# Kernel optimization log

Measured on AMD Instinct MI355X. Metric: run time of the kernel, lower is better.

## Reference

```python
import jax, jax.numpy as jnp
import numpy as np

# PyTorch LSTM cell with zero initial (h, c): W_hh @ h0 == 0, and c = sigmoid(i)*tanh(g)
# since the forget-gate term f*c0 vanishes. Gate order in torch: i, f, g, o.
# b here is the combined b_ih + b_hh (identical math).

def lstm_step0(x, Wih, b):
    pre = x @ Wih.T + b                      # (N, 4H)
    i, f, g, o = jnp.split(pre, 4, axis=-1)
    c = jax.nn.sigmoid(i) * jnp.tanh(g)
    return jax.nn.sigmoid(o) * jnp.tanh(c)   # (N, H)


def setup_inputs() -> dict:
    key = jax.random.key(0)
    ks = jax.random.split(key, 13)
    num_ts, num_periods, F = 128, 256, 128
    GH, NH, NF = 512, 256, 10
    s = lambda k, shape, fan: (jax.random.normal(k, shape, jnp.float32) / np.sqrt(fan))
    return {
        "X": jax.random.normal(ks[0], (num_ts, num_periods, F), jnp.float32),
        "g_Wih0": s(ks[1], (4 * GH, F), F),
        "g_b0": s(ks[2], (4 * GH,), GH),
        "g_Wih1": s(ks[3], (4 * GH, GH), GH),
        "g_b1": s(ks[4], (4 * GH,), GH),
        "aff_W": s(ks[5], (NF, GH), GH),
        "aff_b": s(ks[6], (NF,), GH),
        "n_Wih0": s(ks[7], (4 * NH, F), F),
        "n_b0": s(ks[8], (4 * NH,), NH),
        "n_Wih1": s(ks[9], (4 * NH, NH), NH),
        "n_b1": s(ks[10], (4 * NH,), NH),
        "noise_W": s(ks[11], (1, NH), NH),
        "noise_b": s(ks[12], (1,), NH),
    }


def reference(X, g_Wih0, g_b0, g_Wih1, g_b1, aff_W, aff_b,
              n_Wih0, n_b0, n_Wih1, n_b1, noise_W, noise_b):
    num_ts, num_periods, num_feats = X.shape
    x = X.reshape(-1, num_feats)             # (num_ts*num_periods, F)

    # Global factor branch: 2-layer LSTM single step from zero state
    hg = lstm_step0(lstm_step0(x, g_Wih0, g_b0), g_Wih1, g_b1)
    hg = jax.nn.relu(hg)
    mus = (hg @ aff_W.T + aff_b).sum(axis=-1).reshape(num_ts, num_periods)

    # Noise branch: 2-layer LSTM single step from zero state
    hn = lstm_step0(lstm_step0(x, n_Wih0, n_b0), n_Wih1, n_b1)
    hn = jax.nn.relu(hn)
    sigmas = jax.nn.softplus(hn @ noise_W.T + noise_b)  # log(1+exp(.)), stable
    sigmas = sigmas.reshape(num_ts, num_periods) + 1e-6
    return mus, sigmas
```

## Files before the change

kernel.cpp:

```cpp
#include <hip/hip_runtime.h>
#include <hip/hip_bf16.h>
#include <hip/hip_fp16.h>

typedef _Float16 h8_t __attribute__((ext_vector_type(8)));
typedef _Float16 h4_t __attribute__((ext_vector_type(4)));
typedef float f4_t __attribute__((ext_vector_type(4)));

#define M_ROWS 32768

__device__ __forceinline__ void gload_lds16(const void* g, void* l) {
  __builtin_amdgcn_global_load_lds((const __attribute__((address_space(1))) void*)g,
                                   (__attribute__((address_space(3))) void*)l, 16, 0, 0);
}

__device__ __forceinline__ float sigmoid_f(float x) { return 1.f / (1.f + __expf(-x)); }
__device__ __forceinline__ float tanh_f(float x) { return 1.f - 2.f / (__expf(2.f * x) + 1.f); }

__global__ void cvt_f32_f16(const float* __restrict__ s, _Float16* __restrict__ d, int n) {
  int i = blockIdx.x * blockDim.x + threadIdx.x;
  int i4 = i * 4;
  if (i4 >= n) return;
  float4 v = *(const float4*)(s + i4);
  h4_t o;
  o[0] = (_Float16)v.x; o[1] = (_Float16)v.y; o[2] = (_Float16)v.z; o[3] = (_Float16)v.w;
  *(h4_t*)(d + i4) = o;
}

__global__ void prep_wsum(const float* __restrict__ aff_W, const float* __restrict__ aff_b,
                          float* __restrict__ wsum) {
  int j = threadIdx.x;
  float s = 0.f;
#pragma unroll
  for (int r = 0; r < 10; ++r) s += aff_W[r * 512 + j];
  wsum[j] = s;
  if (j == 0) {
    float bs = 0.f;
#pragma unroll
    for (int r = 0; r < 10; ++r) bs += aff_b[r];
    wsum[512] = bs;
  }
}

__global__ void zero2(float* __restrict__ pg, float* __restrict__ pn) {
  int i = blockIdx.x * blockDim.x + threadIdx.x;
  pg[i] = 0.f;
  pn[i] = 0.f;
}

template <int K_DIM, int H_DIM, bool FUSE>
__global__ __launch_bounds__(256, 2) void lstm_gemm(
    const _Float16* __restrict__ A,
    const _Float16* __restrict__ W,
    const float* __restrict__ bias,
    _Float16* __restrict__ Hout,
    const float* __restrict__ rvec,
    float* __restrict__ partial) {
  __shared__ __align__(16) _Float16 As[128 * 64];
  __shared__ __align__(16) _Float16 Bs[3 * 64 * 64];

  const int tid = threadIdx.x;
  const int wid = tid >> 6;
  const int lane = tid & 63;
  const int wave_m = wid >> 1;
  const int wave_h = wid & 1;
  const int q = lane >> 4;
  const int tcol = lane & 15;

  const int m0 = blockIdx.x * 128;
  const int h0 = blockIdx.y * 64;

  f4_t acc[3][4][2];
#pragma unroll
  for (int p = 0; p < 3; ++p)
#pragma unroll
    for (int mi = 0; mi < 4; ++mi)
#pragma unroll
      for (int ni = 0; ni < 2; ++ni) acc[p][mi][ni] = (f4_t){0.f, 0.f, 0.f, 0.f};

  for (int k0 = 0; k0 < K_DIM; k0 += 64) {
#pragma unroll
    for (int c = 0; c < 4; ++c) {
      int o = ((wid * 4 + c) << 10) + (lane << 4);
      int row = o >> 7;
      int kel = (o & 127) >> 1;
      gload_lds16(A + (size_t)(m0 + row) * K_DIM + k0 + kel, (char*)As + o);
    }
#pragma unroll
    for (int c = 0; c < 6; ++c) {
      int o = ((wid * 6 + c) << 10) + (lane << 4);
      int p = o >> 13;
      int oo = o & 8191;
      int j = oo >> 7;
      int kel = (oo & 127) >> 1;
      int grow = (p == 0 ? 0 : (p == 1 ? 2 * H_DIM : 3 * H_DIM)) + h0 + j;
      gload_lds16(W + (size_t)grow * K_DIM + k0 + kel, (char*)Bs + o);
    }
    __syncthreads();

#pragma unroll
    for (int ks = 0; ks < 2; ++ks) {
      h8_t af[4];
#pragma unroll
      for (int mi = 0; mi < 4; ++mi)
        af[mi] = *(const h8_t*)&As[(wave_m * 64 + mi * 16 + tcol) * 64 + ks * 32 + q * 8];
#pragma unroll
      for (int p = 0; p < 3; ++p) {
#pragma unroll
        for (int ni = 0; ni < 2; ++ni) {
          h8_t bf = *(const h8_t*)&Bs[p * 4096 + (wave_h * 32 + ni * 16 + tcol) * 64 + ks * 32 + q * 8];
#pragma unroll
          for (int mi = 0; mi < 4; ++mi)
            acc[p][mi][ni] = __builtin_amdgcn_mfma_f32_16x16x32_f16(af[mi], bf, acc[p][mi][ni], 0, 0, 0);
        }
      }
    }
    __syncthreads();
  }

  const int mrow0 = m0 + wave_m * 64;
  const int jcol0 = h0 + wave_h * 32;

  if constexpr (!FUSE) {
#pragma unroll
    for (int ni = 0; ni < 2; ++ni) {
      int j = jcol0 + ni * 16 + tcol;
      float bi = bias[j];
      float bg = bias[2 * H_DIM + j];
      float bo = bias[3 * H_DIM + j];
#pragma unroll
      for (int mi = 0; mi < 4; ++mi) {
#pragma unroll
        for (int r = 0; r < 4; ++r) {
          float pi = acc[0][mi][ni][r] + bi;
          float pgt = acc[1][mi][ni][r] + bg;
          float po = acc[2][mi][ni][r] + bo;
          float cc = sigmoid_f(pi) * tanh_f(pgt);
          float hh = sigmoid_f(po) * tanh_f(cc);
          int m = mrow0 + mi * 16 + q * 4 + r;
          Hout[(size_t)m * H_DIM + j] = (_Float16)hh;
        }
      }
    }
  } else {
    float rsum[4][4];
#pragma unroll
    for (int mi = 0; mi < 4; ++mi)
#pragma unroll
      for (int r = 0; r < 4; ++r) rsum[mi][r] = 0.f;
#pragma unroll
    for (int ni = 0; ni < 2; ++ni) {
      int j = jcol0 + ni * 16 + tcol;
      float bi = bias[j];
      float bg = bias[2 * H_DIM + j];
      float bo = bias[3 * H_DIM + j];
      float rv = rvec[j];
#pragma unroll
      for (int mi = 0; mi < 4; ++mi) {
#pragma unroll
        for (int r = 0; r < 4; ++r) {
          float pi = acc[0][mi][ni][r] + bi;
          float pgt = acc[1][mi][ni][r] + bg;
          float po = acc[2][mi][ni][r] + bo;
          float cc = sigmoid_f(pi) * tanh_f(pgt);
          float hh = sigmoid_f(po) * tanh_f(cc);
          hh = fmaxf(hh, 0.f);
          rsum[mi][r] += hh * rv;
        }
      }
    }
#pragma unroll
    for (int mi = 0; mi < 4; ++mi) {
#pragma unroll
      for (int r = 0; r < 4; ++r) {
        float v = rsum[mi][r];
        v += __shfl_xor(v, 1);
        v += __shfl_xor(v, 2);
        v += __shfl_xor(v, 4);
        v += __shfl_xor(v, 8);
        if (tcol == 0) atomicAdd(&partial[mrow0 + mi * 16 + q * 4 + r], v);
      }
    }
  }
}

__global__ void finalize(const float* __restrict__ pg, const float* __restrict__ pn,
                         const float* __restrict__ wsum, const float* __restrict__ noise_b,
                         float* __restrict__ out) {
  int i = blockIdx.x * blockDim.x + threadIdx.x;
  out[i] = pg[i] + wsum[512];
  float x = pn[i] + noise_b[0];
  float sp = fmaxf(x, 0.f) + log1pf(expf(-fabsf(x)));
  out[M_ROWS + i] = sp + 1e-6f;
}

extern "C" void kernel_launch(void* const* d_in, const int* in_sizes, int n_in,
                              void* d_out, int out_size, void* d_ws, size_t ws_size,
                              hipStream_t stream) {
  const float* X       = (const float*)d_in[0];
  const float* g_Wih0  = (const float*)d_in[1];
  const float* g_b0    = (const float*)d_in[2];
  const float* g_Wih1  = (const float*)d_in[3];
  const float* g_b1    = (const float*)d_in[4];
  const float* aff_W   = (const float*)d_in[5];
  const float* aff_b   = (const float*)d_in[6];
  const float* n_Wih0  = (const float*)d_in[7];
  const float* n_b0    = (const float*)d_in[8];
  const float* n_Wih1  = (const float*)d_in[9];
  const float* n_b1    = (const float*)d_in[10];
  const float* noise_W = (const float*)d_in[11];
  const float* noise_b = (const float*)d_in[12];
  float* out = (float*)d_out;

  char* w = (char*)d_ws;
  _Float16* Xh  = (_Float16*)w; w += (size_t)M_ROWS * 128 * 2;
  _Float16* Wg0 = (_Float16*)w; w += 2048 * 128 * 2;
  _Float16* Wg1 = (_Float16*)w; w += 2048 * 512 * 2;
  _Float16* Wn0 = (_Float16*)w; w += 1024 * 128 * 2;
  _Float16* Wn1 = (_Float16*)w; w += 1024 * 256 * 2;
  _Float16* h1g = (_Float16*)w; w += (size_t)M_ROWS * 512 * 2;
  _Float16* h1n = (_Float16*)w; w += (size_t)M_ROWS * 256 * 2;
  float* pg   = (float*)w; w += (size_t)M_ROWS * 4;
  float* pn   = (float*)w; w += (size_t)M_ROWS * 4;
  float* wsum = (float*)w; w += 4096;

  auto cvt = [&](const float* s, _Float16* d, int n) {
    cvt_f32_f16<<<(n / 4 + 255) / 256, 256, 0, stream>>>(s, d, n);
  };
  cvt(X, Xh, M_ROWS * 128);
  cvt(g_Wih0, Wg0, 2048 * 128);
  cvt(g_Wih1, Wg1, 2048 * 512);
  cvt(n_Wih0, Wn0, 1024 * 128);
  cvt(n_Wih1, Wn1, 1024 * 256);
  prep_wsum<<<1, 512, 0, stream>>>(aff_W, aff_b, wsum);
  zero2<<<M_ROWS / 256, 256, 0, stream>>>(pg, pn);

  lstm_gemm<128, 512, false><<<dim3(M_ROWS / 128, 8), 256, 0, stream>>>(Xh, Wg0, g_b0, h1g, nullptr, nullptr);
  lstm_gemm<128, 256, false><<<dim3(M_ROWS / 128, 4), 256, 0, stream>>>(Xh, Wn0, n_b0, h1n, nullptr, nullptr);
  lstm_gemm<512, 512, true><<<dim3(M_ROWS / 128, 8), 256, 0, stream>>>(h1g, Wg1, g_b1, nullptr, wsum, pg);
  lstm_gemm<256, 256, true><<<dim3(M_ROWS / 128, 4), 256, 0, stream>>>(h1n, Wn1, n_b1, nullptr, noise_W, pn);

  finalize<<<M_ROWS / 256, 256, 0, stream>>>(pg, pn, wsum, noise_b, out);
}
```

Baseline: 287.2 us.

## Fuse prep kernels, merge branch GEMMs per layer, swizzle LDS tiles

All preprocessing (f16 casts, accumulator zeroing, affine weight-sum) now runs in one kernel, and the global and noise LSTM GEMMs for each layer are merged into a single launch selected by blockIdx.y. LDS tiles get an XOR swizzle on 16-byte chunks to reduce bank conflicts on the MFMA operand reads. Global pointers are precomputed and bumped each step, and the K loop is fully unrolled. This cuts launch count and tail idle time and may improve LDS throughput, at the cost of more registers and branch divergence across blocks.

```diff
diff --git a/kernel.cpp b/kernel.cpp
--- a/kernel.cpp
+++ b/kernel.cpp
@@ -16,48 +16,59 @@
 __device__ __forceinline__ float sigmoid_f(float x) { return 1.f / (1.f + __expf(-x)); }
 __device__ __forceinline__ float tanh_f(float x) { return 1.f - 2.f / (__expf(2.f * x) + 1.f); }
 
-__global__ void cvt_f32_f16(const float* __restrict__ s, _Float16* __restrict__ d, int n) {
-  int i = blockIdx.x * blockDim.x + threadIdx.x;
-  int i4 = i * 4;
-  if (i4 >= n) return;
+struct GArgs {
+  const _Float16* A;
+  const _Float16* W;
+  const float* bias;
+  _Float16* Hout;
+  const float* rvec;
+  float* partial;
+};
+
+__global__ void prep_all(const float* __restrict__ X, const float* __restrict__ gW0,
+                         const float* __restrict__ gW1, const float* __restrict__ nW0,
+                         const float* __restrict__ nW1, const float* __restrict__ aff_W,
+                         const float* __restrict__ aff_b,
+                         _Float16* __restrict__ Xh, _Float16* __restrict__ Wg0,
+                         _Float16* __restrict__ Wg1, _Float16* __restrict__ Wn0,
+                         _Float16* __restrict__ Wn1,
+                         float* __restrict__ pg, float* __restrict__ pn,
+                         float* __restrict__ wsum) {
+  int b = blockIdx.x;
+  const float* s; _Float16* d; int base;
+  if (b < 4096)      { s = X;   d = Xh;  base = b; }
+  else if (b < 4352) { s = gW0; d = Wg0; base = b - 4096; }
+  else if (b < 5376) { s = gW1; d = Wg1; base = b - 4352; }
+  else if (b < 5504) { s = nW0; d = Wn0; base = b - 5376; }
+  else if (b < 5760) { s = nW1; d = Wn1; base = b - 5504; }
+  else if (b < 5888) {
+    int i = (b - 5760) * 256 + threadIdx.x;
+    pg[i] = 0.f; pn[i] = 0.f;
+    return;
+  } else {
+    int j = (b - 5888) * 256 + threadIdx.x;
+    float sum = 0.f;
+#pragma unroll
+    for (int r = 0; r < 10; ++r) sum += aff_W[r * 512 + j];
+    wsum[j] = sum;
+    if (j == 0) {
+      float bs = 0.f;
+#pragma unroll
+      for (int r = 0; r < 10; ++r) bs += aff_b[r];
+      wsum[512] = bs;
+    }
+    return;
+  }
+  int i4 = (base * 256 + threadIdx.x) * 4;
   float4 v = *(const float4*)(s + i4);
   h4_t o;
   o[0] = (_Float16)v.x; o[1] = (_Float16)v.y; o[2] = (_Float16)v.z; o[3] = (_Float16)v.w;
   *(h4_t*)(d + i4) = o;
 }
 
-__global__ void prep_wsum(const float* __restrict__ aff_W, const float* __restrict__ aff_b,
-                          float* __restrict__ wsum) {
-  int j = threadIdx.x;
-  float s = 0.f;
-#pragma unroll
-  for (int r = 0; r < 10; ++r) s += aff_W[r * 512 + j];
-  wsum[j] = s;
-  if (j == 0) {
-    float bs = 0.f;
-#pragma unroll
-    for (int r = 0; r < 10; ++r) bs += aff_b[r];
-    wsum[512] = bs;
-  }
-}
-
-__global__ void zero2(float* __restrict__ pg, float* __restrict__ pn) {
-  int i = blockIdx.x * blockDim.x + threadIdx.x;
-  pg[i] = 0.f;
-  pn[i] = 0.f;
-}
-
 template <int K_DIM, int H_DIM, bool FUSE>
-__global__ __launch_bounds__(256, 2) void lstm_gemm(
-    const _Float16* __restrict__ A,
-    const _Float16* __restrict__ W,
-    const float* __restrict__ bias,
-    _Float16* __restrict__ Hout,
-    const float* __restrict__ rvec,
-    float* __restrict__ partial) {
-  __shared__ __align__(16) _Float16 As[128 * 64];
-  __shared__ __align__(16) _Float16 Bs[3 * 64 * 64];
-
+__device__ __forceinline__ void gemm_body(const GArgs& ga, int h0,
+                                          _Float16* As, _Float16* Bs) {
   const int tid = threadIdx.x;
   const int wid = tid >> 6;
   const int lane = tid & 63;
@@ -65,9 +76,46 @@
   const int wave_h = wid & 1;
   const int q = lane >> 4;
   const int tcol = lane & 15;
-
   const int m0 = blockIdx.x * 128;
-  const int h0 = blockIdx.y * 64;
+
+  const _Float16* aptr[4]; int aoff[4];
+#pragma unroll
+  for (int c = 0; c < 4; ++c) {
+    int o = ((wid * 4 + c) << 10) + (lane << 4);
+    int row = o >> 7, pch = (o >> 4) & 7;
+    int lch = pch ^ (row & 7);
+    aptr[c] = ga.A + (size_t)(m0 + row) * K_DIM + lch * 8;
+    aoff[c] = o;
+  }
+  const _Float16* bptr[6]; int boff[6];
+#pragma unroll
+  for (int c = 0; c < 6; ++c) {
+    int o = ((wid * 6 + c) << 10) + (lane << 4);
+    int pan = o >> 13;
+    int row = (o >> 7) & 63, pch = (o >> 4) & 7;
+    int lch = pch ^ (row & 7);
+    int gbase = (pan == 0 ? 0 : (pan == 1 ? 2 * H_DIM : 3 * H_DIM)) + h0 + row;
+    bptr[c] = ga.W + (size_t)gbase * K_DIM + lch * 8;
+    boff[c] = o;
+  }
+  int a_rd[2][4];
+#pragma unroll
+  for (int ks = 0; ks < 2; ++ks)
+#pragma unroll
+    for (int mi = 0; mi < 4; ++mi) {
+      int r = wave_m * 64 + mi * 16 + tcol;
+      int c = ks * 4 + q;
+      a_rd[ks][mi] = r * 64 + (c ^ (r & 7)) * 8;
+    }
+  int b_rd[2][2];
+#pragma unroll
+  for (int ks = 0; ks < 2; ++ks)
+#pragma unroll
+    for (int ni = 0; ni < 2; ++ni) {
+      int j = wave_h * 32 + ni * 16 + tcol;
+      int c = ks * 4 + q;
+      b_rd[ks][ni] = j * 64 + (c ^ (j & 7)) * 8;
+    }
 
   f4_t acc[3][4][2];
 #pragma unroll
@@ -77,37 +125,28 @@
 #pragma unroll
       for (int ni = 0; ni < 2; ++ni) acc[p][mi][ni] = (f4_t){0.f, 0.f, 0.f, 0.f};
 
-  for (int k0 = 0; k0 < K_DIM; k0 += 64) {
-#pragma unroll
-    for (int c = 0; c < 4; ++c) {
-      int o = ((wid * 4 + c) << 10) + (lane << 4);
-      int row = o >> 7;
-      int kel = (o & 127) >> 1;
-      gload_lds16(A + (size_t)(m0 + row) * K_DIM + k0 + kel, (char*)As + o);
-    }
-#pragma unroll
-    for (int c = 0; c < 6; ++c) {
-      int o = ((wid * 6 + c) << 10) + (lane << 4);
-      int p = o >> 13;
-      int oo = o & 8191;
-      int j = oo >> 7;
-      int kel = (oo & 127) >> 1;
-      int grow = (p == 0 ? 0 : (p == 1 ? 2 * H_DIM : 3 * H_DIM)) + h0 + j;
-      gload_lds16(W + (size_t)grow * K_DIM + k0 + kel, (char*)Bs + o);
-    }
+#pragma unroll
+  for (int kk = 0; kk < K_DIM / 64; ++kk) {
+#pragma unroll
+    for (int c = 0; c < 4; ++c) gload_lds16(aptr[c], (char*)As + aoff[c]);
+#pragma unroll
+    for (int c = 0; c < 6; ++c) gload_lds16(bptr[c], (char*)Bs + boff[c]);
+#pragma unroll
+    for (int c = 0; c < 4; ++c) aptr[c] += 64;
+#pragma unroll
+    for (int c = 0; c < 6; ++c) bptr[c] += 64;
     __syncthreads();
 
 #pragma unroll
     for (int ks = 0; ks < 2; ++ks) {
       h8_t af[4];
 #pragma unroll
-      for (int mi = 0; mi < 4; ++mi)
-        af[mi] = *(const h8_t*)&As[(wave_m * 64 + mi * 16 + tcol) * 64 + ks * 32 + q * 8];
+      for (int mi = 0; mi < 4; ++mi) af[mi] = *(const h8_t*)&As[a_rd[ks][mi]];
 #pragma unroll
       for (int p = 0; p < 3; ++p) {
 #pragma unroll
         for (int ni = 0; ni < 2; ++ni) {
-          h8_t bf = *(const h8_t*)&Bs[p * 4096 + (wave_h * 32 + ni * 16 + tcol) * 64 + ks * 32 + q * 8];
+          h8_t bf = *(const h8_t*)&Bs[p * 4096 + b_rd[ks][ni]];
 #pragma unroll
           for (int mi = 0; mi < 4; ++mi)
             acc[p][mi][ni] = __builtin_amdgcn_mfma_f32_16x16x32_f16(af[mi], bf, acc[p][mi][ni], 0, 0, 0);
@@ -124,11 +163,11 @@
 #pragma unroll
     for (int ni = 0; ni < 2; ++ni) {
       int j = jcol0 + ni * 16 + tcol;
-      float bi = bias[j];
-      float bg = bias[2 * H_DIM + j];
-      float bo = bias[3 * H_DIM + j];
-#pragma unroll
-      for (int mi = 0; mi < 4; ++mi) {
+      float bi = ga.bias[j];
+      float bg = ga.bias[2 * H_DIM + j];
+      float bo = ga.bias[3 * H_DIM + j];
+#pragma unroll
+      for (int mi = 0; mi < 4; ++mi)
 #pragma unroll
         for (int r = 0; r < 4; ++r) {
           float pi = acc[0][mi][ni][r] + bi;
@@ -137,9 +176,8 @@
           float cc = sigmoid_f(pi) * tanh_f(pgt);
           float hh = sigmoid_f(po) * tanh_f(cc);
           int m = mrow0 + mi * 16 + q * 4 + r;
-          Hout[(size_t)m * H_DIM + j] = (_Float16)hh;
+          ga.Hout[(size_t)m * H_DIM + j] = (_Float16)hh;
         }
-      }
     }
   } else {
     float rsum[4][4];
@@ -150,12 +188,12 @@
 #pragma unroll
     for (int ni = 0; ni < 2; ++ni) {
       int j = jcol0 + ni * 16 + tcol;
-      float bi = bias[j];
-      float bg = bias[2 * H_DIM + j];
-      float bo = bias[3 * H_DIM + j];
-      float rv = rvec[j];
-#pragma unroll
-      for (int mi = 0; mi < 4; ++mi) {
+      float bi = ga.bias[j];
+      float bg = ga.bias[2 * H_DIM + j];
+      float bo = ga.bias[3 * H_DIM + j];
+      float rv = ga.rvec[j];
+#pragma unroll
+      for (int mi = 0; mi < 4; ++mi)
 #pragma unroll
         for (int r = 0; r < 4; ++r) {
           float pi = acc[0][mi][ni][r] + bi;
@@ -166,10 +204,9 @@
           hh = fmaxf(hh, 0.f);
           rsum[mi][r] += hh * rv;
         }
-      }
-    }
-#pragma unroll
-    for (int mi = 0; mi < 4; ++mi) {
+    }
+#pragma unroll
+    for (int mi = 0; mi < 4; ++mi)
 #pragma unroll
       for (int r = 0; r < 4; ++r) {
         float v = rsum[mi][r];
@@ -177,10 +214,25 @@
         v += __shfl_xor(v, 2);
         v += __shfl_xor(v, 4);
         v += __shfl_xor(v, 8);
-        if (tcol == 0) atomicAdd(&partial[mrow0 + mi * 16 + q * 4 + r], v);
+        if (tcol == 0) atomicAdd(&ga.partial[mrow0 + mi * 16 + q * 4 + r], v);
       }
-    }
-  }
+  }
+}
+
+__global__ __launch_bounds__(256, 2) void layer1_fused(GArgs g, GArgs n) {
+  __shared__ __align__(16) _Float16 As[128 * 64];
+  __shared__ __align__(16) _Float16 Bs[3 * 64 * 64];
+  int y = blockIdx.y;
+  if (y < 8) gemm_body<128, 512, false>(g, y * 64, As, Bs);
+  else       gemm_body<128, 256, false>(n, (y - 8) * 64, As, Bs);
+}
+
+__global__ __launch_bounds__(256, 2) void layer2_fused(GArgs g, GArgs n) {
+  __shared__ __align__(16) _Float16 As[128 * 64];
+  __shared__ __align__(16) _Float16 Bs[3 * 64 * 64];
+  int y = blockIdx.y;
+  if (y < 8) gemm_body<512, 512, true>(g, y * 64, As, Bs);
+  else       gemm_body<256, 256, true>(n, (y - 8) * 64, As, Bs);
 }
 
 __global__ void finalize(const float* __restrict__ pg, const float* __restrict__ pn,
@@ -223,21 +275,16 @@
   float* pn   = (float*)w; w += (size_t)M_ROWS * 4;
   float* wsum = (float*)w; w += 4096;
 
-  auto cvt = [&](const float* s, _Float16* d, int n) {
-    cvt_f32_f16<<<(n / 4 + 255) / 256, 256, 0, stream>>>(s, d, n);
-  };
-  cvt(X, Xh, M_ROWS * 128);
-  cvt(g_Wih0, Wg0, 2048 * 128);
-  cvt(g_Wih1, Wg1, 2048 * 512);
-  cvt(n_Wih0, Wn0, 1024 * 128);
-  cvt(n_Wih1, Wn1, 1024 * 256);
-  prep_wsum<<<1, 512, 0, stream>>>(aff_W, aff_b, wsum);
-  zero2<<<M_ROWS / 256, 256, 0, stream>>>(pg, pn);
-
-  lstm_gemm<128, 512, false><<<dim3(M_ROWS / 128, 8), 256, 0, stream>>>(Xh, Wg0, g_b0, h1g, nullptr, nullptr);
-  lstm_gemm<128, 256, false><<<dim3(M_ROWS / 128, 4), 256, 0, stream>>>(Xh, Wn0, n_b0, h1n, nullptr, nullptr);
-  lstm_gemm<512, 512, true><<<dim3(M_ROWS / 128, 8), 256, 0, stream>>>(h1g, Wg1, g_b1, nullptr, wsum, pg);
-  lstm_gemm<256, 256, true><<<dim3(M_ROWS / 128, 4), 256, 0, stream>>>(h1n, Wn1, n_b1, nullptr, noise_W, pn);
+  prep_all<<<5890, 256, 0, stream>>>(X, g_Wih0, g_Wih1, n_Wih0, n_Wih1, aff_W, aff_b,
+                                     Xh, Wg0, Wg1, Wn0, Wn1, pg, pn, wsum);
+
+  GArgs l1g = {Xh, Wg0, g_b0, h1g, nullptr, nullptr};
+  GArgs l1n = {Xh, Wn0, n_b0, h1n, nullptr, nullptr};
+  layer1_fused<<<dim3(M_ROWS / 128, 12), 256, 0, stream>>>(l1g, l1n);
+
+  GArgs l2g = {h1g, Wg1, g_b1, nullptr, wsum, pg};
+  GArgs l2n = {h1n, Wn1, n_b1, nullptr, noise_W, pn};
+  layer2_fused<<<dim3(M_ROWS / 128, 12), 256, 0, stream>>>(l2g, l2n);
 
   finalize<<<M_ROWS / 256, 256, 0, stream>>>(pg, pn, wsum, noise_b, out);
 }
```

After: 262.8 us. -8.5%, faster.
